# Kernel optimization log

Measured on AMD Instinct MI355X. Metric: run time of the kernel, lower is better.

The kernel has to match this reference:

```python
import jax, jax.numpy as jnp
import numpy as np

OBS_DIM, N_CODE, CODE_DIM, H = 32, 512, 16, 256


def _mlp_params(key, sizes):
    ps = {}
    for i, (fin, fout) in enumerate(zip(sizes[:-1], sizes[1:])):
        key, k = jax.random.split(key)
        ps[f'W{i}'] = jax.random.normal(k, (fin, fout), jnp.float32) / np.sqrt(fin)
        ps[f'b{i}'] = jnp.zeros((fout,), jnp.float32)
    return ps


def setup_inputs() -> dict:
    key = jax.random.key(0)
    k_obs, k_enc, k_dec, k_cb = jax.random.split(key, 4)
    enc = _mlp_params(k_enc, [1 + OBS_DIM, H, H, CODE_DIM])
    dec = _mlp_params(k_dec, [CODE_DIM * OBS_DIM, H, H, OBS_DIM])
    return {
        'obs': jax.random.normal(k_obs, (8192, OBS_DIM), jnp.float32),
        'enc_W0': enc['W0'], 'enc_b0': enc['b0'],
        'enc_W1': enc['W1'], 'enc_b1': enc['b1'],
        'enc_W2': enc['W2'], 'enc_b2': enc['b2'],
        'dec_W0': dec['W0'], 'dec_b0': dec['b0'],
        'dec_W1': dec['W1'], 'dec_b1': dec['b1'],
        'dec_W2': dec['W2'], 'dec_b2': dec['b2'],
        'codebook': jax.random.normal(k_cb, (N_CODE, CODE_DIM), jnp.float32),
    }


def _mlp(x, W0, b0, W1, b1, W2, b2):
    h = jax.nn.relu(x @ W0 + b0)
    h = jax.nn.relu(h @ W1 + b1)
    return h @ W2 + b2


def _quantize(emb, codebook):
    # emb: [N, D], codebook: [K, D]. Nearest-neighbor by squared L2.
    d = (jnp.sum(emb * emb, -1, keepdims=True)
         - 2.0 * emb @ codebook.T
         + jnp.sum(codebook * codebook, -1))  # [N, K]
    idx = jnp.argmin(d, axis=-1)              # [N]
    q = codebook[idx]                          # gather [N, D]
    # straight-through estimator
    return emb + jax.lax.stop_gradient(q - emb)


def reference(obs, enc_W0, enc_b0, enc_W1, enc_b1, enc_W2, enc_b2,
              dec_W0, dec_b0, dec_W1, dec_b1, dec_W2, dec_b2, codebook):
    B = obs.shape[0]
    x = obs[:, :, None]                                        # [B, O, 1]
    eye = jnp.eye(OBS_DIM, dtype=obs.dtype)                    # [O, O]
    onehot = jnp.broadcast_to(eye, (B, OBS_DIM, OBS_DIM))
    enc_in = jnp.concatenate([x, onehot], axis=-1)             # [B, O, 1+O]
    emb = _mlp(enc_in, enc_W0, enc_b0, enc_W1, enc_b1, enc_W2, enc_b2)  # [B, O, D]
    q = _quantize(emb.reshape(B * OBS_DIM, CODE_DIM), codebook)
    q = q.reshape(B, OBS_DIM * CODE_DIM)
    recon = _mlp(q, dec_W0, dec_b0, dec_W1, dec_b1, dec_W2, dec_b2)     # [B, O]
    return recon
```

## Files before the change

kernel.cpp:

```cpp
#include <hip/hip_runtime.h>

#define OBS   32
#define NC    512
#define CD    16
#define HD    256
#define BATCH 8192
#define EPS   4e-3f

typedef unsigned short u16;
typedef unsigned int   u32;
typedef __attribute__((ext_vector_type(8))) short bf16x8;
typedef __attribute__((ext_vector_type(4))) float f32x4;

__device__ __forceinline__ short f2bf(float x) {
    union { float f; u32 u; } v; v.f = x;
    u32 r = (v.u + 0x7fffu + ((v.u >> 16) & 1u)) >> 16;
    return (short)r;
}
__device__ __forceinline__ float bf2f(short s) {
    union { u32 u; float f; } v; v.u = ((u32)(u16)s) << 16; return v.f;
}

__global__ void prep_kernel(const float* __restrict__ cb,
                            const float* __restrict__ W1,
                            const float* __restrict__ W2,
                            const float* __restrict__ W0,
                            const float* __restrict__ B0,
                            float* __restrict__ n32, double* __restrict__ n64,
                            int* __restrict__ fcnt,
                            u16* __restrict__ wsW1, u16* __restrict__ wsW2,
                            u16* __restrict__ wsCB, float* __restrict__ w0m) {
    const int b = blockIdx.x, t = threadIdx.x;
    if (b == 0) {
        if (t == 0) *fcnt = 0;
        #pragma unroll
        for (int h = 0; h < 2; ++h) {
            int c = t + h * 256;
            const float* r = cb + c * CD;
            float s32 = 0.f; double s64 = 0.0;
            #pragma unroll
            for (int j = 0; j < CD; ++j) {
                float v = r[j];
                s32 = fmaf(v, v, s32);
                s64 = fma((double)v, (double)v, s64);
            }
            n32[c] = s32; n64[c] = s64;
        }
    } else if (b <= 256) {
        int e = (b - 1) * 256 + t;
        int k = e >> 8, n = e & 255;
        float w = W1[k * 256 + n];
        short hi = f2bf(w);
        short lo = f2bf(w - bf2f(hi));
        int s = k >> 5, koff = k & 31;
        wsW1[s * 16384 + n * 32 + koff]        = (u16)hi;
        wsW1[s * 16384 + 8192 + n * 32 + koff] = (u16)lo;
    } else if (b == 257) {
        #pragma unroll
        for (int i = 0; i < 16; ++i) {
            int e = t * 16 + i;
            int k = e >> 4, n = e & 15;
            float w = W2[k * CD + n];
            short hi = f2bf(w);
            short lo = f2bf(w - bf2f(hi));
            wsW2[n * 264 + k]        = (u16)hi;
            wsW2[4224 + n * 264 + k] = (u16)lo;
        }
    } else if (b == 258) {
        #pragma unroll
        for (int i = 0; i < 8; ++i) {
            int sl = t * 8 + i;
            int tile = sl >> 6, l = sl & 63;
            int n  = tile * 16 + (l & 15);
            int kb = ((l >> 4) & 1) * 8;
            u16* dh = wsCB + tile * 1024 + l * 8;
            u16* dl = dh + 512;
            #pragma unroll
            for (int j = 0; j < 8; ++j) {
                float w = cb[n * CD + kb + j];
                short hi = f2bf(w);
                dh[j] = (u16)hi;
                dl[j] = (u16)f2bf(w - bf2f(hi));
            }
        }
    } else {
        #pragma unroll
        for (int m = 0; m < OBS; ++m)
            w0m[m * HD + t] = W0[(1 + m) * HD + t] + B0[t];
    }
}

__global__ void __launch_bounds__(256) encoder_kernel(
    const float* __restrict__ obs,
    const float* __restrict__ W0, const float* __restrict__ w0m,
    const float* __restrict__ B1, const float* __restrict__ B2,
    const u16* __restrict__ wsW1, const u16* __restrict__ wsW2,
    const u16* __restrict__ wsCB, const float* __restrict__ n32,
    int* __restrict__ idxbuf, int* __restrict__ fcnt, int* __restrict__ flist)
{
    __shared__ __align__(16) u16   hH[32 * 264];
    __shared__ __align__(16) u16   hL[32 * 264];
    __shared__ __align__(16) float embs[OBS * CD];
    __shared__ float redD[4][OBS][2];
    __shared__ int   redI[4][OBS][2];

    const int tid = threadIdx.x;
    const int blk = blockIdx.x;
    const int l   = tid & 63;
    const int wv  = tid >> 6;
    const int q   = l >> 4;
    const int ln  = l & 15;
    const int nq  = wv;

    if (wv < 2) {
        const int m = wv * 16 + ln;
        const float x = obs[blk * OBS + m];
        const float* W0m = w0m + m * HD;
        #pragma unroll
        for (int s = 0; s < 8; ++s) {
            const int k0 = s * 32 + q * 8;
            float w0v[8], wmv[8];
            *(float4*)&w0v[0] = *(const float4*)(W0 + k0);
            *(float4*)&w0v[4] = *(const float4*)(W0 + k0 + 4);
            *(float4*)&wmv[0] = *(const float4*)(W0m + k0);
            *(float4*)&wmv[4] = *(const float4*)(W0m + k0 + 4);
            u32 hiP[4], loP[4];
            #pragma unroll
            for (int jp = 0; jp < 4; ++jp) {
                float ha = fmaxf(fmaf(x, w0v[2 * jp],     wmv[2 * jp]),     0.f);
                float hb = fmaxf(fmaf(x, w0v[2 * jp + 1], wmv[2 * jp + 1]), 0.f);
                short h0 = f2bf(ha), h1 = f2bf(hb);
                short l0 = f2bf(ha - bf2f(h0)), l1 = f2bf(hb - bf2f(h1));
                hiP[jp] = ((u32)(u16)h1 << 16) | (u32)(u16)h0;
                loP[jp] = ((u32)(u16)l1 << 16) | (u32)(u16)l0;
            }
            *(uint4*)&hH[m * 264 + k0] = *(uint4*)&hiP[0];
            *(uint4*)&hL[m * 264 + k0] = *(uint4*)&loP[0];
        }
    }
    __syncthreads();

    f32x4 acc[2][4];
    #pragma unroll
    for (int mt = 0; mt < 2; ++mt)
        #pragma unroll
        for (int nt = 0; nt < 4; ++nt) acc[mt][nt] = (f32x4){0.f, 0.f, 0.f, 0.f};

    {
        const u16* pB = wsW1 + (nq * 64 + ln) * 32 + q * 8;
        #pragma unroll
        for (int s = 0; s < 8; ++s) {
            bf16x8 AH[2], AL[2];
            #pragma unroll
            for (int mt = 0; mt < 2; ++mt) {
                const int ao = (mt * 16 + ln) * 264 + s * 32 + q * 8;
                AH[mt] = *(const bf16x8*)&hH[ao];
                AL[mt] = *(const bf16x8*)&hL[ao];
            }
            const u16* ph = pB + s * 16384;
            const u16* pl = ph + 8192;
            #pragma unroll
            for (int nt = 0; nt < 4; ++nt) {
                bf16x8 Bh = *(const bf16x8*)(ph + nt * 512);
                bf16x8 Bl = *(const bf16x8*)(pl + nt * 512);
                #pragma unroll
                for (int mt = 0; mt < 2; ++mt) {
                    f32x4 a = acc[mt][nt];
                    a = __builtin_amdgcn_mfma_f32_16x16x32_bf16(AH[mt], Bh, a, 0, 0, 0);
                    a = __builtin_amdgcn_mfma_f32_16x16x32_bf16(AH[mt], Bl, a, 0, 0, 0);
                    a = __builtin_amdgcn_mfma_f32_16x16x32_bf16(AL[mt], Bh, a, 0, 0, 0);
                    acc[mt][nt] = a;
                }
            }
        }
    }
    __syncthreads();

    {
        #pragma unroll
        for (int nt = 0; nt < 4; ++nt) {
            const int n = nq * 64 + nt * 16 + ln;
            const float b1 = B1[n];
            #pragma unroll
            for (int mt = 0; mt < 2; ++mt) {
                #pragma unroll
                for (int r = 0; r < 4; ++r) {
                    float h = fmaxf(acc[mt][nt][r] + b1, 0.f);
                    short hi = f2bf(h);
                    short lo = f2bf(h - bf2f(hi));
                    const int mr = mt * 16 + q * 4 + r;
                    hH[mr * 264 + n] = (u16)hi;
                    hL[mr * 264 + n] = (u16)lo;
                }
            }
        }
    }
    __syncthreads();

    if (wv < 2) {
        f32x4 ac = (f32x4){0.f, 0.f, 0.f, 0.f};
        const int abase = (wv * 16 + ln) * 264 + q * 8;
        const u16* pWh = wsW2 + ln * 264 + q * 8;
        const u16* pWl = pWh + 4224;
        #pragma unroll
        for (int s = 0; s < 8; ++s) {
            bf16x8 Ah2 = *(const bf16x8*)&hH[abase + s * 32];
            bf16x8 Al2 = *(const bf16x8*)&hL[abase + s * 32];
            bf16x8 Bh  = *(const bf16x8*)(pWh + s * 32);
            bf16x8 Bl  = *(const bf16x8*)(pWl + s * 32);
            ac = __builtin_amdgcn_mfma_f32_16x16x32_bf16(Ah2, Bh, ac, 0, 0, 0);
            ac = __builtin_amdgcn_mfma_f32_16x16x32_bf16(Ah2, Bl, ac, 0, 0, 0);
            ac = __builtin_amdgcn_mfma_f32_16x16x32_bf16(Al2, Bh, ac, 0, 0, 0);
        }
        const float b2 = B2[ln];
        #pragma unroll
        for (int r = 0; r < 4; ++r)
            embs[(wv * 16 + q * 4 + r) * CD + ln] = ac[r] + b2;
    }
    __syncthreads();

    {
        bf16x8 Ae[2];
        #pragma unroll
        for (int ms = 0; ms < 2; ++ms) {
            const float* ep = embs + (ms * 16 + ln) * CD + (q & 1) * 8;
            float4 ea = *(const float4*)ep;
            float4 eb = *(const float4*)(ep + 4);
            float ev[8] = { ea.x, ea.y, ea.z, ea.w, eb.x, eb.y, eb.z, eb.w };
            #pragma unroll
            for (int j = 0; j < 8; ++j) {
                short hi = f2bf(ev[j]);
                Ae[ms][j] = (q < 2) ? hi : f2bf(ev[j] - bf2f(hi));
            }
        }
        float d1[2][4], d2[2][4]; int i1[2][4], i2[2][4];
        #pragma unroll
        for (int ms = 0; ms < 2; ++ms)
            #pragma unroll
            for (int r = 0; r < 4; ++r) {
                d1[ms][r] = d2[ms][r] = 3.4e38f;
                i1[ms][r] = i2[ms][r] = 0x7fffffff;
            }

        const u16* pC = wsCB + (wv * 8) * 1024 + l * 8;
        #pragma unroll
        for (int tb = 0; tb < 8; ++tb) {
            const u16* pt = pC + tb * 1024;
            bf16x8 Bh = *(const bf16x8*)pt;
            bf16x8 Bl = *(const bf16x8*)(pt + 512);
            const int ci = (wv * 8 + tb) * 16 + ln;
            const float cn = n32[ci];
            #pragma unroll
            for (int ms = 0; ms < 2; ++ms) {
                f32x4 a = (f32x4){0.f, 0.f, 0.f, 0.f};
                a = __builtin_amdgcn_mfma_f32_16x16x32_bf16(Ae[ms], Bh, a, 0, 0, 0);
                a = __builtin_amdgcn_mfma_f32_16x16x32_bf16(Ae[ms], Bl, a, 0, 0, 0);
                #pragma unroll
                for (int r = 0; r < 4; ++r) {
                    float d = fmaf(-2.f, a[r], cn);
                    if (d < d1[ms][r]) {
                        d2[ms][r] = d1[ms][r]; i2[ms][r] = i1[ms][r];
                        d1[ms][r] = d; i1[ms][r] = ci;
                    } else if (d < d2[ms][r]) { d2[ms][r] = d; i2[ms][r] = ci; }
                }
            }
        }
        #pragma unroll
        for (int off = 8; off >= 1; off >>= 1) {
            #pragma unroll
            for (int ms = 0; ms < 2; ++ms)
                #pragma unroll
                for (int r = 0; r < 4; ++r) {
                    float od1 = __shfl_down(d1[ms][r], off, 16);
                    int   oi1 = __shfl_down(i1[ms][r], off, 16);
                    float od2 = __shfl_down(d2[ms][r], off, 16);
                    int   oi2 = __shfl_down(i2[ms][r], off, 16);
                    bool ob = (od1 < d1[ms][r]) ||
                              (od1 == d1[ms][r] && oi1 < i1[ms][r]);
                    float n1d, n2d; int n1i, n2i;
                    if (ob) {
                        n1d = od1; n1i = oi1;
                        bool t2 = (d1[ms][r] < od2) ||
                                  (d1[ms][r] == od2 && i1[ms][r] < oi2);
                        n2d = t2 ? d1[ms][r] : od2; n2i = t2 ? i1[ms][r] : oi2;
                    } else {
                        n1d = d1[ms][r]; n1i = i1[ms][r];
                        bool t2 = (od1 < d2[ms][r]) ||
                                  (od1 == d2[ms][r] && oi1 < i2[ms][r]);
                        n2d = t2 ? od1 : d2[ms][r]; n2i = t2 ? oi1 : i2[ms][r];
                    }
                    d1[ms][r] = n1d; i1[ms][r] = n1i;
                    d2[ms][r] = n2d; i2[ms][r] = n2i;
                }
        }
        if (ln == 0) {
            #pragma unroll
            for (int ms = 0; ms < 2; ++ms)
                #pragma unroll
                for (int r = 0; r < 4; ++r) {
                    const int m = ms * 16 + q * 4 + r;
                    redD[wv][m][0] = d1[ms][r]; redD[wv][m][1] = d2[ms][r];
                    redI[wv][m][0] = i1[ms][r]; redI[wv][m][1] = i2[ms][r];
                }
        }
    }
    __syncthreads();

    if (tid < OBS) {
        const int m = tid;
        float d1 = redD[0][m][0], d2 = redD[0][m][1];
        int   i1 = redI[0][m][0], i2 = redI[0][m][1];
        #pragma unroll
        for (int h = 1; h < 4; ++h) {
            #pragma unroll
            for (int e = 0; e < 2; ++e) {
                float db = redD[h][m][e]; int ib = redI[h][m][e];
                if (db < d1 || (db == d1 && ib < i1)) {
                    d2 = d1; i2 = i1; d1 = db; i1 = ib;
                } else if (db < d2 || (db == d2 && ib < i2)) { d2 = db; i2 = ib; }
            }
        }
        const int T = blk * OBS + m;
        idxbuf[T] = i1;
        if (d2 - d1 < EPS) {
            int pos = atomicAdd(fcnt, 1);
            flist[pos] = T;
        }
    }
}

__global__ void __launch_bounds__(256) fixup_kernel(
    const float* __restrict__ obs,
    const float* __restrict__ W0, const float* __restrict__ B0,
    const float* __restrict__ W1, const float* __restrict__ B1,
    const float* __restrict__ W2, const float* __restrict__ B2,
    const float* __restrict__ cb, const double* __restrict__ n64,
    const int* __restrict__ fcnt, const int* __restrict__ flist,
    int* __restrict__ idxbuf)
{
    __shared__ double h0s[HD];
    __shared__ double h1s[HD];
    __shared__ double ep[16][17];
    __shared__ double es[CD];
    __shared__ double dmin[256];
    __shared__ int    imin[256];

    int n = *fcnt;
    if (n > BATCH * OBS) n = BATCH * OBS;
    const int j = threadIdx.x;

    for (int f = blockIdx.x; f < n; f += gridDim.x) {
        const int T = flist[f];
        const int b = T >> 5, t = T & 31;
        const double x = (double)obs[b * OBS + t];
        {
            double a = fma(x, (double)W0[j], (double)W0[(1 + t) * HD + j])
                     + (double)B0[j];
            h0s[j] = a > 0.0 ? a : 0.0;
        }
        __syncthreads();
        {
            double s = 0.0;
            for (int k = 0; k < HD; ++k)
                s = fma(h0s[k], (double)W1[k * HD + j], s);
            s += (double)B1[j];
            h1s[j] = s > 0.0 ? s : 0.0;
        }
        __syncthreads();
        {
            const int d = j & 15, part = j >> 4;
            double s = 0.0;
            for (int k = part * 16; k < part * 16 + 16; ++k)
                s = fma(h1s[k], (double)W2[k * CD + d], s);
            ep[part][d] = s;
        }
        __syncthreads();
        if (j < CD) {
            double s = 0.0;
            for (int p = 0; p < 16; ++p) s += ep[p][j];
            es[j] = s + (double)B2[j];
        }
        __syncthreads();
        {
            double best = 1e300; int bi = 0x7fffffff;
            for (int c = j; c < NC; c += 256) {
                double dot = 0.0;
                #pragma unroll
                for (int qq = 0; qq < CD; ++qq)
                    dot = fma(es[qq], (double)cb[c * CD + qq], dot);
                double D = n64[c] - 2.0 * dot;
                if (D < best || (D == best && c < bi)) { best = D; bi = c; }
            }
            dmin[j] = best; imin[j] = bi;
        }
        __syncthreads();
        if (j == 0) {
            double best = dmin[0]; int bi = imin[0];
            for (int k = 1; k < 256; ++k)
                if (dmin[k] < best || (dmin[k] == best && imin[k] < bi)) {
                    best = dmin[k]; bi = imin[k];
                }
            idxbuf[T] = bi;
        }
        __syncthreads();
    }
}

__global__ void __launch_bounds__(256) decoder_kernel(
    const int* __restrict__ idx, const float* __restrict__ cbk,
    const float* __restrict__ W0, const float* __restrict__ B0,
    const float* __restrict__ W1, const float* __restrict__ B1,
    const float* __restrict__ W2, const float* __restrict__ B2,
    float* __restrict__ out)
{
    __shared__ float qb[16][512];
    __shared__ float hb[16][256];
    const int tid = threadIdx.x;
    const int row0 = blockIdx.x * 16;

    {
        const int base = row0 * OBS;
        #pragma unroll
        for (int m = 0; m < 2; ++m) {
            int g = tid * 2 + m;
            int ciq = idx[base + g];
            const float4* src = (const float4*)(cbk + ciq * CD);
            float4* dst = (float4*)&qb[g >> 5][(g & 31) * CD];
            dst[0] = src[0]; dst[1] = src[1]; dst[2] = src[2]; dst[3] = src[3];
        }
    }
    __syncthreads();

    const int jg = tid & 63, tg = tid >> 6;
    const int j0 = jg * 4, r0 = tg * 4;

    {
        float acA[4][4], acB[4][4];
        #pragma unroll
        for (int tt = 0; tt < 4; ++tt)
            #pragma unroll
            for (int u = 0; u < 4; ++u) { acA[tt][u] = 0.f; acB[tt][u] = 0.f; }
        for (int k = 0; k < 512; k += 4) {
            float hr[4][4];
            #pragma unroll
            for (int tt = 0; tt < 4; ++tt) {
                float4 hv = *(const float4*)&qb[r0 + tt][k];
                hr[tt][0] = hv.x; hr[tt][1] = hv.y; hr[tt][2] = hv.z; hr[tt][3] = hv.w;
            }
            #pragma unroll
            for (int p = 0; p < 4; ++p) {
                float4 w = *(const float4*)(W0 + (k + p) * 256 + j0);
                if (p < 2) {
                    #pragma unroll
                    for (int tt = 0; tt < 4; ++tt) {
                        acA[tt][0] = fmaf(hr[tt][p], w.x, acA[tt][0]);
                        acA[tt][1] = fmaf(hr[tt][p], w.y, acA[tt][1]);
                        acA[tt][2] = fmaf(hr[tt][p], w.z, acA[tt][2]);
                        acA[tt][3] = fmaf(hr[tt][p], w.w, acA[tt][3]);
                    }
                } else {
                    #pragma unroll
                    for (int tt = 0; tt < 4; ++tt) {
                        acB[tt][0] = fmaf(hr[tt][p], w.x, acB[tt][0]);
                        acB[tt][1] = fmaf(hr[tt][p], w.y, acB[tt][1]);
                        acB[tt][2] = fmaf(hr[tt][p], w.z, acB[tt][2]);
                        acB[tt][3] = fmaf(hr[tt][p], w.w, acB[tt][3]);
                    }
                }
            }
        }
        #pragma unroll
        for (int tt = 0; tt < 4; ++tt)
            #pragma unroll
            for (int u = 0; u < 4; ++u)
                hb[r0 + tt][j0 + u] = fmaxf((acA[tt][u] + acB[tt][u]) + B0[j0 + u], 0.f);
    }
    __syncthreads();

    float* h2 = &qb[0][0];
    {
        float acA[4][4], acB[4][4];
        #pragma unroll
        for (int tt = 0; tt < 4; ++tt)
            #pragma unroll
            for (int u = 0; u < 4; ++u) { acA[tt][u] = 0.f; acB[tt][u] = 0.f; }
        for (int k = 0; k < 256; k += 4) {
            float hr[4][4];
            #pragma unroll
            for (int tt = 0; tt < 4; ++tt) {
                float4 hv = *(const float4*)&hb[r0 + tt][k];
                hr[tt][0] = hv.x; hr[tt][1] = hv.y; hr[tt][2] = hv.z; hr[tt][3] = hv.w;
            }
            #pragma unroll
            for (int p = 0; p < 4; ++p) {
                float4 w = *(const float4*)(W1 + (k + p) * 256 + j0);
                if (p < 2) {
                    #pragma unroll
                    for (int tt = 0; tt < 4; ++tt) {
                        acA[tt][0] = fmaf(hr[tt][p], w.x, acA[tt][0]);
                        acA[tt][1] = fmaf(hr[tt][p], w.y, acA[tt][1]);
                        acA[tt][2] = fmaf(hr[tt][p], w.z, acA[tt][2]);
                        acA[tt][3] = fmaf(hr[tt][p], w.w, acA[tt][3]);
                    }
                } else {
                    #pragma unroll
                    for (int tt = 0; tt < 4; ++tt) {
                        acB[tt][0] = fmaf(hr[tt][p], w.x, acB[tt][0]);
                        acB[tt][1] = fmaf(hr[tt][p], w.y, acB[tt][1]);
                        acB[tt][2] = fmaf(hr[tt][p], w.z, acB[tt][2]);
                        acB[tt][3] = fmaf(hr[tt][p], w.w, acB[tt][3]);
                    }
                }
            }
        }
        __syncthreads();
        #pragma unroll
        for (int tt = 0; tt < 4; ++tt)
            #pragma unroll
            for (int u = 0; u < 4; ++u)
                h2[(r0 + tt) * 256 + j0 + u] =
                    fmaxf((acA[tt][u] + acB[tt][u]) + B1[j0 + u], 0.f);
    }
    __syncthreads();

    {
        const int c  = tid & 31;
        const int rg = tid >> 5;
        for (int rr = rg; rr < 16; rr += 8) {
            float a0 = 0.f, a1 = 0.f, a2 = 0.f, a3 = 0.f;
            #pragma unroll 4
            for (int k = 0; k < 256; k += 4) {
                float4 hv = *(const float4*)&h2[rr * 256 + k];
                a0 = fmaf(hv.x, W2[(k + 0) * 32 + c], a0);
                a1 = fmaf(hv.y, W2[(k + 1) * 32 + c], a1);
                a2 = fmaf(hv.z, W2[(k + 2) * 32 + c], a2);
                a3 = fmaf(hv.w, W2[(k + 3) * 32 + c], a3);
            }
            out[(row0 + rr) * 32 + c] = ((a0 + a1) + (a2 + a3)) + B2[c];
        }
    }
}

extern "C" void kernel_launch(void* const* d_in, const int* in_sizes, int n_in,
                              void* d_out, int out_size, void* d_ws, size_t ws_size,
                              hipStream_t stream) {
    (void)in_sizes; (void)n_in; (void)out_size; (void)ws_size;
    const float* obs = (const float*)d_in[0];
    const float* eW0 = (const float*)d_in[1];
    const float* eb0 = (const float*)d_in[2];
    const float* eW1 = (const float*)d_in[3];
    const float* eb1 = (const float*)d_in[4];
    const float* eW2 = (const float*)d_in[5];
    const float* eb2 = (const float*)d_in[6];
    const float* dW0 = (const float*)d_in[7];
    const float* db0 = (const float*)d_in[8];
    const float* dW1 = (const float*)d_in[9];
    const float* db1 = (const float*)d_in[10];
    const float* dW2 = (const float*)d_in[11];
    const float* db2 = (const float*)d_in[12];
    const float* cb  = (const float*)d_in[13];

    char*   ws    = (char*)d_ws;
    float*  n32   = (float*)ws;
    double* n64   = (double*)(ws + 4096);
    int*    fcnt  = (int*)(ws + 8192);
    int*    flist = (int*)(ws + 8448);
    int*    idxb  = (int*)(ws + 8448 + 1048576);
    float*  w0m   = (float*)(ws + 3145728);
    u16*    wsW1  = (u16*)(ws + 4194304);
    u16*    wsW2  = (u16*)(ws + 4194304 + 262144);
    u16*    wsCB  = (u16*)(ws + 4194304 + 262144 + 32768);

    prep_kernel<<<260, 256, 0, stream>>>(cb, eW1, eW2, eW0, eb0, n32, n64, fcnt,
                                         wsW1, wsW2, wsCB, w0m);
    encoder_kernel<<<BATCH, 256, 0, stream>>>(obs, eW0, w0m, eb1, eb2,
                                              wsW1, wsW2, wsCB, n32,
                                              idxb, fcnt, flist);
    fixup_kernel<<<256, 256, 0, stream>>>(obs, eW0, eb0, eW1, eb1, eW2, eb2,
                                          cb, n64, fcnt, flist, idxb);
    decoder_kernel<<<BATCH / 16, 256, 0, stream>>>(idxb, cb, dW0, db0, dW1, db1,
                                                   dW2, db2, (float*)d_out);
}
```

Baseline: 425.9 us.

## Streamline encoder: branchless top-2 search, precomputed bf16 emb splits, all-thread layer-0

Layer-0 hidden computation is spread over all 256 threads instead of two waves. Embeddings are split into bf16 hi/lo once when written rather than re-split on every read. The nearest-code search now tracks only the second-best distance, not its index, using branchless fmin/fmax updates in the scan, the shuffle reduction and the cross-wave merge. Codebook norms are loaded up front, which trims divergence and register pressure in the argmin loop.

```diff
diff --git a/kernel.cpp b/kernel.cpp
--- a/kernel.cpp
+++ b/kernel.cpp
@@ -98,11 +98,12 @@
     const u16* __restrict__ wsCB, const float* __restrict__ n32,
     int* __restrict__ idxbuf, int* __restrict__ fcnt, int* __restrict__ flist)
 {
-    __shared__ __align__(16) u16   hH[32 * 264];
-    __shared__ __align__(16) u16   hL[32 * 264];
-    __shared__ __align__(16) float embs[OBS * CD];
+    __shared__ __align__(16) u16  hH[32 * 264];
+    __shared__ __align__(16) u16  hL[32 * 264];
+    __shared__ __align__(16) u16  embsH[32 * 24];
+    __shared__ __align__(16) u16  embsL[32 * 24];
     __shared__ float redD[4][OBS][2];
-    __shared__ int   redI[4][OBS][2];
+    __shared__ int   redI[4][OBS];
 
     const int tid = threadIdx.x;
     const int blk = blockIdx.x;
@@ -112,13 +113,14 @@
     const int ln  = l & 15;
     const int nq  = wv;
 
-    if (wv < 2) {
-        const int m = wv * 16 + ln;
+    {
+        const int m = tid >> 3;
+        const int p = tid & 7;
         const float x = obs[blk * OBS + m];
         const float* W0m = w0m + m * HD;
         #pragma unroll
-        for (int s = 0; s < 8; ++s) {
-            const int k0 = s * 32 + q * 8;
+        for (int s = 0; s < 4; ++s) {
+            const int k0 = s * 64 + p * 8;
             float w0v[8], wmv[8];
             *(float4*)&w0v[0] = *(const float4*)(W0 + k0);
             *(float4*)&w0v[4] = *(const float4*)(W0 + k0 + 4);
@@ -214,32 +216,34 @@
         }
         const float b2 = B2[ln];
         #pragma unroll
-        for (int r = 0; r < 4; ++r)
-            embs[(wv * 16 + q * 4 + r) * CD + ln] = ac[r] + b2;
-    }
-    __syncthreads();
-
-    {
+        for (int r = 0; r < 4; ++r) {
+            float e = ac[r] + b2;
+            short hi = f2bf(e);
+            short lo = f2bf(e - bf2f(hi));
+            const int row = wv * 16 + q * 4 + r;
+            embsH[row * 24 + ln] = (u16)hi;
+            embsL[row * 24 + ln] = (u16)lo;
+        }
+    }
+    __syncthreads();
+
+    {
+        const u16* ebase = (q < 2) ? embsH : embsL;
         bf16x8 Ae[2];
-        #pragma unroll
-        for (int ms = 0; ms < 2; ++ms) {
-            const float* ep = embs + (ms * 16 + ln) * CD + (q & 1) * 8;
-            float4 ea = *(const float4*)ep;
-            float4 eb = *(const float4*)(ep + 4);
-            float ev[8] = { ea.x, ea.y, ea.z, ea.w, eb.x, eb.y, eb.z, eb.w };
-            #pragma unroll
-            for (int j = 0; j < 8; ++j) {
-                short hi = f2bf(ev[j]);
-                Ae[ms][j] = (q < 2) ? hi : f2bf(ev[j] - bf2f(hi));
-            }
-        }
-        float d1[2][4], d2[2][4]; int i1[2][4], i2[2][4];
+        Ae[0] = *(const bf16x8*)&ebase[(ln)      * 24 + (q & 1) * 8];
+        Ae[1] = *(const bf16x8*)&ebase[(16 + ln) * 24 + (q & 1) * 8];
+
+        float cn8[8];
+        #pragma unroll
+        for (int tb = 0; tb < 8; ++tb) cn8[tb] = n32[(wv * 8 + tb) * 16 + ln];
+
+        float d1[2][4], d2[2][4]; int i1[2][4];
         #pragma unroll
         for (int ms = 0; ms < 2; ++ms)
             #pragma unroll
             for (int r = 0; r < 4; ++r) {
                 d1[ms][r] = d2[ms][r] = 3.4e38f;
-                i1[ms][r] = i2[ms][r] = 0x7fffffff;
+                i1[ms][r] = 0x7fffffff;
             }
 
         const u16* pC = wsCB + (wv * 8) * 1024 + l * 8;
@@ -249,7 +253,6 @@
             bf16x8 Bh = *(const bf16x8*)pt;
             bf16x8 Bl = *(const bf16x8*)(pt + 512);
             const int ci = (wv * 8 + tb) * 16 + ln;
-            const float cn = n32[ci];
             #pragma unroll
             for (int ms = 0; ms < 2; ++ms) {
                 f32x4 a = (f32x4){0.f, 0.f, 0.f, 0.f};
@@ -257,11 +260,11 @@
                 a = __builtin_amdgcn_mfma_f32_16x16x32_bf16(Ae[ms], Bl, a, 0, 0, 0);
                 #pragma unroll
                 for (int r = 0; r < 4; ++r) {
-                    float d = fmaf(-2.f, a[r], cn);
-                    if (d < d1[ms][r]) {
-                        d2[ms][r] = d1[ms][r]; i2[ms][r] = i1[ms][r];
-                        d1[ms][r] = d; i1[ms][r] = ci;
-                    } else if (d < d2[ms][r]) { d2[ms][r] = d; i2[ms][r] = ci; }
+                    float d = fmaf(-2.f, a[r], cn8[tb]);
+                    bool lt = d < d1[ms][r];
+                    d2[ms][r] = fminf(d2[ms][r], fmaxf(d1[ms][r], d));
+                    d1[ms][r] = fminf(d1[ms][r], d);
+                    i1[ms][r] = lt ? ci : i1[ms][r];
                 }
             }
         }
@@ -274,23 +277,12 @@
                     float od1 = __shfl_down(d1[ms][r], off, 16);
                     int   oi1 = __shfl_down(i1[ms][r], off, 16);
                     float od2 = __shfl_down(d2[ms][r], off, 16);
-                    int   oi2 = __shfl_down(i2[ms][r], off, 16);
                     bool ob = (od1 < d1[ms][r]) ||
                               (od1 == d1[ms][r] && oi1 < i1[ms][r]);
-                    float n1d, n2d; int n1i, n2i;
-                    if (ob) {
-                        n1d = od1; n1i = oi1;
-                        bool t2 = (d1[ms][r] < od2) ||
-                                  (d1[ms][r] == od2 && i1[ms][r] < oi2);
-                        n2d = t2 ? d1[ms][r] : od2; n2i = t2 ? i1[ms][r] : oi2;
-                    } else {
-                        n1d = d1[ms][r]; n1i = i1[ms][r];
-                        bool t2 = (od1 < d2[ms][r]) ||
-                                  (od1 == d2[ms][r] && oi1 < i2[ms][r]);
-                        n2d = t2 ? od1 : d2[ms][r]; n2i = t2 ? oi1 : i2[ms][r];
-                    }
-                    d1[ms][r] = n1d; i1[ms][r] = n1i;
-                    d2[ms][r] = n2d; i2[ms][r] = n2i;
+                    float hi2 = fmaxf(d1[ms][r], od1);
+                    d1[ms][r] = fminf(d1[ms][r], od1);
+                    i1[ms][r] = ob ? oi1 : i1[ms][r];
+                    d2[ms][r] = fminf(fminf(d2[ms][r], od2), hi2);
                 }
         }
         if (ln == 0) {
@@ -300,7 +292,7 @@
                 for (int r = 0; r < 4; ++r) {
                     const int m = ms * 16 + q * 4 + r;
                     redD[wv][m][0] = d1[ms][r]; redD[wv][m][1] = d2[ms][r];
-                    redI[wv][m][0] = i1[ms][r]; redI[wv][m][1] = i2[ms][r];
+                    redI[wv][m] = i1[ms][r];
                 }
         }
     }
@@ -309,16 +301,16 @@
     if (tid < OBS) {
         const int m = tid;
         float d1 = redD[0][m][0], d2 = redD[0][m][1];
-        int   i1 = redI[0][m][0], i2 = redI[0][m][1];
+        int   i1 = redI[0][m];
         #pragma unroll
         for (int h = 1; h < 4; ++h) {
-            #pragma unroll
-            for (int e = 0; e < 2; ++e) {
-                float db = redD[h][m][e]; int ib = redI[h][m][e];
-                if (db < d1 || (db == d1 && ib < i1)) {
-                    d2 = d1; i2 = i1; d1 = db; i1 = ib;
-                } else if (db < d2 || (db == d2 && ib < i2)) { d2 = db; i2 = ib; }
-            }
+            float a1 = redD[h][m][0], a2 = redD[h][m][1];
+            int   ai = redI[h][m];
+            bool ob = (a1 < d1) || (a1 == d1 && ai < i1);
+            float hi2 = fmaxf(d1, a1);
+            d1 = fminf(d1, a1);
+            i1 = ob ? ai : i1;
+            d2 = fminf(fminf(d2, a2), hi2);
         }
         const int T = blk * OBS + m;
         idxbuf[T] = i1;
```

After: 374.3 us. 1.14x faster.
